# Kernel tuning notes

Hardware: AMD Instinct MI355X
Metric: run time of the kernel (lower is better)

The kernel has to match this reference:

```python
import jax, jax.numpy as jnp
from jax import lax
import numpy as np

B, C, H, W_SP = 2, 64, 80, 80
IC = C // 2  # inter_channels = 32


def _conv3x3(x, w, b):
    # x: (b,c,h,w), w: (o,c,3,3), padding=1 -> SAME
    y = lax.conv_general_dilated(x, w, (1, 1), 'SAME',
                                 dimension_numbers=('NCHW', 'OIHW', 'NCHW'))
    return y + b[None, :, None, None]


def setup_inputs() -> dict:
    key = jax.random.key(0)
    ks = jax.random.split(key, 8)
    x = jax.random.normal(ks[0], (B, C, H, W_SP), dtype=jnp.float32)
    x_t = jax.random.normal(ks[1], (B, C, H, W_SP), dtype=jnp.float32)
    # learned parameters (random, fan-in scaled; W is zero-init in the original
    # module but we use random weights so the op is numerically non-trivial)
    g_w = jax.random.normal(ks[2], (IC, C, 1, 1), dtype=jnp.float32) / np.sqrt(C)
    g_b = jax.random.normal(ks[3], (IC,), dtype=jnp.float32) * 0.01
    W_w = jax.random.normal(ks[4], (C, IC, 1, 1), dtype=jnp.float32) / np.sqrt(IC)
    W_b = jax.random.normal(ks[5], (C,), dtype=jnp.float32) * 0.01
    shared_w = jax.random.normal(ks[6], (IC, C, 3, 3), dtype=jnp.float32) / np.sqrt(9 * C)
    shared_b = jax.random.normal(ks[7], (IC,), dtype=jnp.float32) * 0.01
    return {'x': x, 'x_t': x_t, 'g_w': g_w, 'g_b': g_b,
            'W_w': W_w, 'W_b': W_b, 'shared_w': shared_w, 'shared_b': shared_b}


def reference(x, x_t, g_w, g_b, W_w, W_b, shared_w, shared_b):
    b, c, h, w = x.shape
    ic = g_w.shape[0]
    n = h * w  # flattened spatial positions
    # g: 1x1 conv on x_t -> (b, n, ic)
    g_x_t = jnp.einsum('oc,bchw->bohw', g_w[:, :, 0, 0], x_t) + g_b[None, :, None, None]
    g_x_t = g_x_t.reshape(b, ic, n).transpose(0, 2, 1)
    # shared 3x3 conv for theta (on x) and phi (on x_t)
    theta_x = _conv3x3(x, shared_w, shared_b).reshape(b, ic, n).transpose(0, 2, 1)  # (b,n,ic)
    phi_x_t = _conv3x3(x_t, shared_w, shared_b).reshape(b, ic, n)                    # (b,ic,n)
    # unscaled dot-product attention over spatial positions
    f = jnp.einsum('bnc,bcm->bnm', theta_x, phi_x_t)  # (b,n,n)
    f_div_C = jax.nn.softmax(f, axis=-1)
    y = jnp.einsum('bnm,bmc->bnc', f_div_C, g_x_t)    # (b,n,ic)
    y = y.transpose(0, 2, 1).reshape(b, ic, h, w)
    # W: 1x1 conv back to in_channels, residual add
    W_y = jnp.einsum('oc,bchw->bohw', W_w[:, :, 0, 0], y) + W_b[None, :, None, None]
    return W_y + x
```

## Files before the change

kernel.cpp:

```cpp
#include <hip/hip_runtime.h>

typedef __attribute__((ext_vector_type(8))) _Float16 half8;
typedef __attribute__((ext_vector_type(4))) _Float16 half4;
typedef __attribute__((ext_vector_type(4))) float f32x4;

#define NB 2
#define CIN 64
#define ICH 32
#define HH 80
#define WW 80
#define NSP 6400
#define KSPLIT 5
#define KRANGE 1280
#define KBLK 128
#define NITER 10
#define QBLK 32
#define QGROUPS 50

__global__ __launch_bounds__(256) void nlb_trans_kernel(
    const float* __restrict__ x, const float* __restrict__ x_t,
    const float* __restrict__ shared_w, const float* __restrict__ g_w,
    _Float16* __restrict__ Xf16, _Float16* __restrict__ W9f,
    _Float16* __restrict__ GWf)
{
    const int bid = blockIdx.x;
    const int tid = threadIdx.x;

    if (bid >= 320) {
        int e = (bid - 320) * 256 + tid;
        if (e < 9 * 32 * 64) {
            int c = e & 63, o = (e >> 6) & 31, tap = e >> 11;
            W9f[e] = (_Float16)shared_w[(o * 64 + c) * 9 + tap];
        } else {
            int e2 = e - 9 * 32 * 64;
            GWf[e2] = (_Float16)g_w[e2];
        }
        return;
    }

    const int src = bid & 1;
    const int b   = (bid >> 1) & 1;
    const int h   = bid >> 2;
    const float* __restrict__ in = src ? x_t : x;

    __shared__ float ts[CIN][WW + 1];

    #pragma unroll
    for (int i = 0; i < 5; ++i) {
        int idx = tid + i * 256;
        int c = idx / 20, w4 = idx % 20;
        float4 v = *(const float4*)(in + ((size_t)(b * CIN + c) * HH + h) * WW + w4 * 4);
        ts[c][w4 * 4 + 0] = v.x;
        ts[c][w4 * 4 + 1] = v.y;
        ts[c][w4 * 4 + 2] = v.z;
        ts[c][w4 * 4 + 3] = v.w;
    }
    __syncthreads();

    _Float16* __restrict__ dst = Xf16 + ((size_t)(src * NB + b) * NSP + h * WW) * CIN;
    #pragma unroll
    for (int i = 0; i < 3; ++i) {
        int idx = tid + i * 256;
        if (idx < 640) {
            int w = idx >> 3, cb = idx & 7;
            half8 o;
            #pragma unroll
            for (int k = 0; k < 8; ++k) o[k] = (_Float16)ts[cb * 8 + k][w];
            *(half8*)(dst + (size_t)w * CIN + cb * 8) = o;
        }
    }
}

__global__ __launch_bounds__(256) void nlb_conv_mfma_kernel(
    const _Float16* __restrict__ Xf16,
    const _Float16* __restrict__ W9f, const _Float16* __restrict__ GWf,
    const float* __restrict__ shared_b, const float* __restrict__ g_b,
    _Float16* __restrict__ Q, _Float16* __restrict__ K, _Float16* __restrict__ Vt)
{
    const int bid = blockIdx.x;
    const int src = bid & 1;
    const int b   = (bid >> 1) & 1;
    const int h   = bid >> 2;

    __shared__ _Float16 xs[3 * 82 * 64];

    const int tid = threadIdx.x;
    const _Float16* __restrict__ Xb = Xf16 + (size_t)(src * NB + b) * NSP * CIN;

    #pragma unroll
    for (int i = 0; i < 8; ++i) {
        int idx = tid + i * 256;
        if (idx < 1920) {
            int rr = idx / 640;
            int rem = idx % 640;
            int w  = rem >> 3, cb = rem & 7;
            int wi = w + 1;
            int hr = h + rr - 1;
            half8 v = {};
            if (hr >= 0 && hr < HH)
                v = *(const half8*)(Xb + ((size_t)(hr * WW + w)) * CIN + cb * 8);
            int slot = cb ^ ((wi + (wi >> 3)) & 7);
            *(half8*)(&xs[(rr * 82 + wi) * 64 + slot * 8]) = v;
        }
    }
    if (tid < 48) {
        int cb = tid & 7;
        int wi = ((tid >> 3) & 1) ? 81 : 0;
        int rr = tid >> 4;
        int slot = cb ^ ((wi + (wi >> 3)) & 7);
        half8 z = {};
        *(half8*)(&xs[(rr * 82 + wi) * 64 + slot * 8]) = z;
    }
    __syncthreads();

    const int wid  = tid >> 6;
    const int lane = tid & 63;
    const int g = lane >> 4, r = lane & 15;
    const int o0 = (wid & 1) * 16;
    const int ti_lo = (wid >> 1) ? 3 : 0;
    const int ti_hi = (wid >> 1) ? 5 : 3;

    half8 aw[9][2];
    #pragma unroll
    for (int tap = 0; tap < 9; ++tap)
        #pragma unroll
        for (int ch = 0; ch < 2; ++ch)
            aw[tap][ch] = *(const half8*)(W9f + ((tap * 32 + o0 + r) * 64 + ch * 32 + g * 8));
    half8 gaf[2];
    if (src) {
        #pragma unroll
        for (int ch = 0; ch < 2; ++ch)
            gaf[ch] = *(const half8*)(GWf + ((o0 + r) * 64 + ch * 32 + g * 8));
    }

    f32x4 biasv, gbv = {0.f, 0.f, 0.f, 0.f};
    #pragma unroll
    for (int j = 0; j < 4; ++j) biasv[j] = shared_b[o0 + g * 4 + j];
    if (src) {
        #pragma unroll
        for (int j = 0; j < 4; ++j) gbv[j] = g_b[o0 + g * 4 + j];
    }

    for (int ti = ti_lo; ti < ti_hi; ++ti) {
        const int n0 = ti * 16;
        const int wi0 = n0 + r;
        f32x4 accE = biasv;
        f32x4 accO = {0.f, 0.f, 0.f, 0.f};
        f32x4 vacc = gbv;
        #pragma unroll
        for (int tap = 0; tap < 9; ++tap) {
            const int kh = tap / 3, kw = tap % 3;
            const int wi = wi0 + kw;
            const int swz = (wi + (wi >> 3)) & 7;
            #pragma unroll
            for (int ch = 0; ch < 2; ++ch) {
                half8 bf = *(const half8*)(&xs[(kh * 82 + wi) * 64 + (((ch * 4 + g) ^ swz) * 8)]);
                if (tap & 1) accO = __builtin_amdgcn_mfma_f32_16x16x32_f16(aw[tap][ch], bf, accO, 0, 0, 0);
                else         accE = __builtin_amdgcn_mfma_f32_16x16x32_f16(aw[tap][ch], bf, accE, 0, 0, 0);
                if (src && tap == 4)
                    vacc = __builtin_amdgcn_mfma_f32_16x16x32_f16(gaf[ch], bf, vacc, 0, 0, 0);
            }
        }
        const int n = h * WW + n0 + r;
        f32x4 acc;
        #pragma unroll
        for (int j = 0; j < 4; ++j) acc[j] = accE[j] + accO[j];
        half4 pk;
        #pragma unroll
        for (int j = 0; j < 4; ++j) pk[j] = (_Float16)acc[j];
        if (!src) {
            *(half4*)(Q + (size_t)(b * NSP + n) * ICH + o0 + g * 4) = pk;
        } else {
            *(half4*)(K + (size_t)(b * NSP + n) * ICH + o0 + g * 4) = pk;
            #pragma unroll
            for (int j = 0; j < 4; ++j)
                Vt[(size_t)(b * ICH + o0 + g * 4 + j) * NSP + n] = (_Float16)vacc[j];
        }
    }
}

#define KPAD 40
#define VPAD 136

__global__ __launch_bounds__(256) void nlb_attn_kernel(
    const _Float16* __restrict__ Q, const _Float16* __restrict__ Km,
    const _Float16* __restrict__ Vt,
    float* __restrict__ YU, float* __restrict__ ML)
{
    const int bid = blockIdx.x;
    const int tg  = bid % QGROUPS;
    const int rem = bid / QGROUPS;
    const int b = rem & 1;
    const int s = rem >> 1;

    const int tid  = threadIdx.x;
    const int wid  = tid >> 6;
    const int lane = tid & 63;
    const int g = lane >> 4, r = lane & 15;

    __shared__ __align__(16) _Float16 Kls[2][KBLK][KPAD];
    __shared__ __align__(16) _Float16 Vls[2][ICH][VPAD];

    const _Float16* __restrict__ Qb = Q  + (size_t)b * NSP * ICH;
    const _Float16* __restrict__ Kb = Km + (size_t)b * NSP * ICH + (size_t)s * KRANGE * ICH;
    const _Float16* __restrict__ Vb = Vt + (size_t)b * ICH * NSP + s * KRANGE;

    const f32x4 zero4 = {0.f, 0.f, 0.f, 0.f};

    const int q0 = tg * 128 + wid * QBLK;
    half8 qa[2];
    #pragma unroll
    for (int qf = 0; qf < 2; ++qf)
        qa[qf] = *(const half8*)(Qb + (size_t)(q0 + qf * 16 + r) * ICH + g * 8);

    f32x4 yacc[2][2];
    float m2[2], lp[2];
    #pragma unroll
    for (int qf = 0; qf < 2; ++qf) {
        yacc[qf][0] = zero4; yacc[qf][1] = zero4;
        m2[qf] = -1e30f; lp[qf] = 0.f;
    }

    const int ka_r = tid >> 2,          ka_c = tid & 3;
    const int kb_r = (tid + 256) >> 2,  kb_c = (tid + 256) & 3;
    const int va_r = tid >> 4,          va_c = tid & 15;
    const int vb_r = (tid + 256) >> 4,  vb_c = (tid + 256) & 15;

    {
        *(half8*)(&Kls[0][ka_r][ka_c * 8]) = *(const half8*)(Kb + (size_t)ka_r * ICH + ka_c * 8);
        *(half8*)(&Kls[0][kb_r][kb_c * 8]) = *(const half8*)(Kb + (size_t)kb_r * ICH + kb_c * 8);
        *(half8*)(&Vls[0][va_r][va_c * 8]) = *(const half8*)(Vb + (size_t)va_r * NSP + va_c * 8);
        *(half8*)(&Vls[0][vb_r][vb_c * 8]) = *(const half8*)(Vb + (size_t)vb_r * NSP + vb_c * 8);
    }
    __syncthreads();

    int cur = 0;
    for (int it = 0; it < NITER; ++it) {
        const bool more = (it + 1 < NITER);
        half8 kst0, kst1, vst0, vst1;
        if (more) {
            const _Float16* Kn = Kb + (size_t)(it + 1) * KBLK * ICH;
            const _Float16* Vn = Vb + (size_t)(it + 1) * KBLK;
            kst0 = *(const half8*)(Kn + (size_t)ka_r * ICH + ka_c * 8);
            kst1 = *(const half8*)(Kn + (size_t)kb_r * ICH + kb_c * 8);
            vst0 = *(const half8*)(Vn + (size_t)va_r * NSP + va_c * 8);
            vst1 = *(const half8*)(Vn + (size_t)vb_r * NSP + vb_c * 8);
        }

        half8 kf[8];
        #pragma unroll
        for (int kh = 0; kh < 8; ++kh)
            kf[kh] = *(const half8*)(&Kls[cur][kh * 16 + r][g * 8]);

        #pragma unroll
        for (int qf = 0; qf < 2; ++qf) {
            f32x4 sa[8];
            __builtin_amdgcn_s_setprio(1);
            #pragma unroll
            for (int kh = 0; kh < 8; ++kh)
                sa[kh] = __builtin_amdgcn_mfma_f32_16x16x32_f16(kf[kh], qa[qf], zero4, 0, 0, 0);
            __builtin_amdgcn_s_setprio(0);

            float vmax = -1e30f;
            #pragma unroll
            for (int kh = 0; kh < 8; ++kh)
                vmax = fmaxf(vmax, fmaxf(fmaxf(sa[kh][0], sa[kh][1]),
                                         fmaxf(sa[kh][2], sa[kh][3])));
            if (__any(vmax - m2[qf] > 8.f)) {
                float tm = vmax;
                tm = fmaxf(tm, __shfl_xor(tm, 16));
                tm = fmaxf(tm, __shfl_xor(tm, 32));
                float mn = fmaxf(m2[qf], tm);
                float sc = __expf(m2[qf] - mn);
                m2[qf] = mn; lp[qf] *= sc;
                #pragma unroll
                for (int j = 0; j < 4; ++j) { yacc[qf][0][j] *= sc; yacc[qf][1][j] *= sc; }
            }

            #pragma unroll
            for (int kh = 0; kh < 8; ++kh) {
                half4 pk; float ls = 0.f;
                #pragma unroll
                for (int j = 0; j < 4; ++j) {
                    float p = __expf(sa[kh][j] - m2[qf]);
                    ls += p; pk[j] = (_Float16)p;
                }
                lp[qf] += ls;
                half4 vfa = *(const half4*)(&Vls[cur][r][kh * 16 + g * 4]);
                half4 vfb = *(const half4*)(&Vls[cur][16 + r][kh * 16 + g * 4]);
                yacc[qf][0] = __builtin_amdgcn_mfma_f32_16x16x16f16(vfa, pk, yacc[qf][0], 0, 0, 0);
                yacc[qf][1] = __builtin_amdgcn_mfma_f32_16x16x16f16(vfb, pk, yacc[qf][1], 0, 0, 0);
            }
        }

        if (more) {
            *(half8*)(&Kls[cur ^ 1][ka_r][ka_c * 8]) = kst0;
            *(half8*)(&Kls[cur ^ 1][kb_r][kb_c * 8]) = kst1;
            *(half8*)(&Vls[cur ^ 1][va_r][va_c * 8]) = vst0;
            *(half8*)(&Vls[cur ^ 1][vb_r][vb_c * 8]) = vst1;
        }
        __syncthreads();
        cur ^= 1;
    }

    #pragma unroll
    for (int qf = 0; qf < 2; ++qf) {
        float lv = lp[qf];
        lv += __shfl_xor(lv, 16);
        lv += __shfl_xor(lv, 32);
        if (g == 0) {
            size_t base = ((size_t)(s * NB + b) * NSP + q0 + qf * 16 + r) * 2;
            ML[base + 0] = m2[qf];
            ML[base + 1] = lv;
        }
        #pragma unroll
        for (int ch = 0; ch < 2; ++ch)
            *(f32x4*)(YU + ((size_t)(s * NB + b) * NSP + q0 + qf * 16 + r) * ICH
                      + ch * 16 + g * 4) = yacc[qf][ch];
    }
}

__global__ __launch_bounds__(256) void nlb_combine_kernel(
    const float* __restrict__ YU, const float* __restrict__ ML,
    const float* __restrict__ W_w, const float* __restrict__ W_b,
    const float* __restrict__ x, float* __restrict__ out)
{
    const int bid = blockIdx.x;
    const int b = bid / 200;
    const int rowbase = (bid % 200) * 32;

    __shared__ float ylds[32][33];
    __shared__ float wwl[CIN * ICH];

    const int tid = threadIdx.x;
    for (int e = tid; e < CIN * ICH; e += 256) wwl[e] = W_w[e];

    #pragma unroll
    for (int i = 0; i < 4; ++i) {
        int idx = tid + i * 256;
        int row = idx >> 5, c = idx & 31;
        int grow = rowbase + row;
        float m[KSPLIT], lv[KSPLIT], M = -1e30f;
        #pragma unroll
        for (int s2 = 0; s2 < KSPLIT; ++s2) {
            size_t base = ((size_t)(s2 * NB + b) * NSP + grow) * 2;
            m[s2]  = ML[base + 0];
            lv[s2] = ML[base + 1];
            M = fmaxf(M, m[s2]);
        }
        float denom = 0.f, acc = 0.f;
        #pragma unroll
        for (int s2 = 0; s2 < KSPLIT; ++s2) {
            float e2 = __expf(m[s2] - M);
            denom += lv[s2] * e2;
            acc += YU[((size_t)(s2 * NB + b) * NSP + grow) * ICH + c] * e2;
        }
        ylds[row][c] = acc / denom;
    }
    __syncthreads();

    const int row = tid & 31;
    const int o0  = tid >> 5;
    #pragma unroll
    for (int k = 0; k < 8; ++k) {
        int o = o0 * 8 + k;
        size_t gi = (size_t)(b * CIN + o) * NSP + rowbase + row;
        float accv = W_b[o] + x[gi];
        #pragma unroll
        for (int c = 0; c < ICH; ++c) accv += wwl[o * ICH + c] * ylds[row][c];
        out[gi] = accv;
    }
}

extern "C" void kernel_launch(void* const* d_in, const int* in_sizes, int n_in,
                              void* d_out, int out_size, void* d_ws, size_t ws_size,
                              hipStream_t stream) {
    const float* x        = (const float*)d_in[0];
    const float* x_t      = (const float*)d_in[1];
    const float* g_w      = (const float*)d_in[2];
    const float* g_b      = (const float*)d_in[3];
    const float* W_w      = (const float*)d_in[4];
    const float* W_b      = (const float*)d_in[5];
    const float* shared_w = (const float*)d_in[6];
    const float* shared_b = (const float*)d_in[7];
    float* out = (float*)d_out;

    char* ws = (char*)d_ws;
    _Float16* Q    = (_Float16*)(ws);
    _Float16* K    = (_Float16*)(ws + 819200);
    _Float16* Vt   = (_Float16*)(ws + 1638400);
    float*    YU   = (float*)(ws + 2457600);
    float*    ML   = (float*)(ws + 10649600);
    _Float16* W9f  = (_Float16*)(ws + 11161600);
    _Float16* GWf  = (_Float16*)(ws + 11198464);
    _Float16* Xf16 = (_Float16*)(ws + 11202560);

    hipLaunchKernelGGL(nlb_trans_kernel, dim3(400), dim3(256), 0, stream,
                       x, x_t, shared_w, g_w, Xf16, W9f, GWf);
    hipLaunchKernelGGL(nlb_conv_mfma_kernel, dim3(320), dim3(256), 0, stream,
                       Xf16, W9f, GWf, shared_b, g_b, Q, K, Vt);
    hipLaunchKernelGGL(nlb_attn_kernel, dim3(NB * QGROUPS * KSPLIT), dim3(256), 0, stream,
                       Q, K, Vt, YU, ML);
    hipLaunchKernelGGL(nlb_combine_kernel, dim3(400), dim3(256), 0, stream,
                       YU, ML, W_w, W_b, x, out);
}
```

Before: 59.76 us.

## Fuse split-K combine into attention kernel via last-block atomic counter

```diff
diff --git a/kernel.cpp b/kernel.cpp
--- a/kernel.cpp
+++ b/kernel.cpp
@@ -182,10 +182,13 @@
 #define KPAD 40
 #define VPAD 136
 
-__global__ __launch_bounds__(256) void nlb_attn_kernel(
+__global__ __launch_bounds__(256) void nlb_attn_fused_kernel(
     const _Float16* __restrict__ Q, const _Float16* __restrict__ Km,
     const _Float16* __restrict__ Vt,
-    float* __restrict__ YU, float* __restrict__ ML)
+    float* __restrict__ YU, float* __restrict__ ML,
+    unsigned* __restrict__ cnt,
+    const float* __restrict__ W_w, const float* __restrict__ W_b,
+    const float* __restrict__ x, float* __restrict__ out)
 {
     const int bid = blockIdx.x;
     const int tg  = bid % QGROUPS;
@@ -198,8 +201,9 @@
     const int lane = tid & 63;
     const int g = lane >> 4, r = lane & 15;
 
-    __shared__ __align__(16) _Float16 Kls[2][KBLK][KPAD];
-    __shared__ __align__(16) _Float16 Vls[2][ICH][VPAD];
+    __shared__ __align__(16) char smem[2 * KBLK * KPAD * 2 + 2 * ICH * VPAD * 2];
+    _Float16 (*Kls)[KBLK][KPAD] = (_Float16 (*)[KBLK][KPAD])smem;
+    _Float16 (*Vls)[ICH][VPAD]  = (_Float16 (*)[ICH][VPAD])(smem + 2 * KBLK * KPAD * 2);
 
     const _Float16* __restrict__ Qb = Q  + (size_t)b * NSP * ICH;
     const _Float16* __restrict__ Kb = Km + (size_t)b * NSP * ICH + (size_t)s * KRANGE * ICH;
@@ -318,57 +322,61 @@
             *(f32x4*)(YU + ((size_t)(s * NB + b) * NSP + q0 + qf * 16 + r) * ICH
                       + ch * 16 + g * 4) = yacc[qf][ch];
     }
-}
-
-__global__ __launch_bounds__(256) void nlb_combine_kernel(
-    const float* __restrict__ YU, const float* __restrict__ ML,
-    const float* __restrict__ W_w, const float* __restrict__ W_b,
-    const float* __restrict__ x, float* __restrict__ out)
-{
-    const int bid = blockIdx.x;
-    const int b = bid / 200;
-    const int rowbase = (bid % 200) * 32;
-
-    __shared__ float ylds[32][33];
-    __shared__ float wwl[CIN * ICH];
-
-    const int tid = threadIdx.x;
+
+    __syncthreads();
+    __shared__ int isLast;
+    if (tid == 0) {
+        __threadfence();
+        unsigned old = atomicAdd(&cnt[b * QGROUPS + tg], 1u);
+        isLast = (old == KSPLIT - 1);
+    }
+    __syncthreads();
+    if (!isLast) return;
+    __threadfence();
+
+    float* wwl        = (float*)smem;
+    float (*ylds)[33] = (float (*)[33])(smem + 8192);
+
     for (int e = tid; e < CIN * ICH; e += 256) wwl[e] = W_w[e];
 
-    #pragma unroll
-    for (int i = 0; i < 4; ++i) {
-        int idx = tid + i * 256;
-        int row = idx >> 5, c = idx & 31;
-        int grow = rowbase + row;
-        float m[KSPLIT], lv[KSPLIT], M = -1e30f;
-        #pragma unroll
-        for (int s2 = 0; s2 < KSPLIT; ++s2) {
-            size_t base = ((size_t)(s2 * NB + b) * NSP + grow) * 2;
-            m[s2]  = ML[base + 0];
-            lv[s2] = ML[base + 1];
-            M = fmaxf(M, m[s2]);
-        }
-        float denom = 0.f, acc = 0.f;
-        #pragma unroll
-        for (int s2 = 0; s2 < KSPLIT; ++s2) {
-            float e2 = __expf(m[s2] - M);
-            denom += lv[s2] * e2;
-            acc += YU[((size_t)(s2 * NB + b) * NSP + grow) * ICH + c] * e2;
-        }
-        ylds[row][c] = acc / denom;
-    }
-    __syncthreads();
-
-    const int row = tid & 31;
-    const int o0  = tid >> 5;
-    #pragma unroll
-    for (int k = 0; k < 8; ++k) {
-        int o = o0 * 8 + k;
-        size_t gi = (size_t)(b * CIN + o) * NSP + rowbase + row;
-        float accv = W_b[o] + x[gi];
-        #pragma unroll
-        for (int c = 0; c < ICH; ++c) accv += wwl[o * ICH + c] * ylds[row][c];
-        out[gi] = accv;
+    const int rowg = tg * 128;
+    for (int chunk = 0; chunk < 4; ++chunk) {
+        const int rowbase = rowg + chunk * 32;
+        __syncthreads();
+        #pragma unroll
+        for (int i = 0; i < 4; ++i) {
+            int idx = tid + i * 256;
+            int row = idx >> 5, c = idx & 31;
+            int grow = rowbase + row;
+            float m[KSPLIT], lv[KSPLIT], M = -1e30f;
+            #pragma unroll
+            for (int s2 = 0; s2 < KSPLIT; ++s2) {
+                size_t base = ((size_t)(s2 * NB + b) * NSP + grow) * 2;
+                m[s2]  = ML[base + 0];
+                lv[s2] = ML[base + 1];
+                M = fmaxf(M, m[s2]);
+            }
+            float denom = 0.f, acc = 0.f;
+            #pragma unroll
+            for (int s2 = 0; s2 < KSPLIT; ++s2) {
+                float e2 = __expf(m[s2] - M);
+                denom += lv[s2] * e2;
+                acc += YU[((size_t)(s2 * NB + b) * NSP + grow) * ICH + c] * e2;
+            }
+            ylds[row][c] = acc / denom;
+        }
+        __syncthreads();
+        const int row = tid & 31;
+        const int o0  = tid >> 5;
+        #pragma unroll
+        for (int k = 0; k < 8; ++k) {
+            int o = o0 * 8 + k;
+            size_t gi = (size_t)(b * CIN + o) * NSP + rowbase + row;
+            float accv = W_b[o] + x[gi];
+            #pragma unroll
+            for (int c = 0; c < 32; ++c) accv += wwl[o * ICH + c] * ylds[row][c];
+            out[gi] = accv;
+        }
     }
 }
 
@@ -394,13 +402,13 @@
     _Float16* W9f  = (_Float16*)(ws + 11161600);
     _Float16* GWf  = (_Float16*)(ws + 11198464);
     _Float16* Xf16 = (_Float16*)(ws + 11202560);
-
+    unsigned* cnt  = (unsigned*)(ws + 14479360);
+
+    hipMemsetAsync(cnt, 0, NB * QGROUPS * sizeof(unsigned), stream);
     hipLaunchKernelGGL(nlb_trans_kernel, dim3(400), dim3(256), 0, stream,
                        x, x_t, shared_w, g_w, Xf16, W9f, GWf);
     hipLaunchKernelGGL(nlb_conv_mfma_kernel, dim3(320), dim3(256), 0, stream,
                        Xf16, W9f, GWf, shared_b, g_b, Q, K, Vt);
-    hipLaunchKernelGGL(nlb_attn_kernel, dim3(NB * QGROUPS * KSPLIT), dim3(256), 0, stream,
-                       Q, K, Vt, YU, ML);
-    hipLaunchKernelGGL(nlb_combine_kernel, dim3(400), dim3(256), 0, stream,
-                       YU, ML, W_w, W_b, x, out);
+    hipLaunchKernelGGL(nlb_attn_fused_kernel, dim3(NB * QGROUPS * KSPLIT), dim3(256), 0, stream,
+                       Q, K, Vt, YU, ML, cnt, W_w, W_b, x, out);
 }
```

Result: slower. 91.40 us (+52.9%).
